# Kernel optimization log

Hardware: AMD Instinct MI355X
Metric: run time of the kernel (lower is better)

Reference implementation:

```python
import jax, jax.numpy as jnp
import numpy as np

P = 2    # padding
R = 2    # ref[0]: rows/cols gathered as conv channels
WP = 3   # ref[1]: conv kernel length along border


def setup_inputs() -> dict:
    key = jax.random.key(0)
    ks = jax.random.split(key, 8)
    B, C, H, W = 8, 128, 256, 256
    HID = 8
    x = jax.random.normal(ks[0], (B, C, H, W), dtype=jnp.float32)
    # stacked params for 4 border MLPs: order top, bottom, left, right
    w1 = jax.random.normal(ks[1], (4, HID, R, WP), dtype=jnp.float32) * 0.3
    b1 = jax.random.normal(ks[2], (4, HID), dtype=jnp.float32) * 0.1
    w2 = jax.random.normal(ks[3], (4, HID, HID), dtype=jnp.float32) * 0.3
    b2 = jax.random.normal(ks[4], (4, HID), dtype=jnp.float32) * 0.1
    w3 = jax.random.normal(ks[5], (4, 1, HID), dtype=jnp.float32) * 0.3
    b3 = jax.random.normal(ks[6], (4, 1), dtype=jnp.float32) * 0.1
    return {"x": x, "w1": w1, "b1": b1, "w2": w2, "b2": b2, "w3": w3, "b3": b3}


def _mlp(slab, w1, b1, w2, b2, w3, b3):
    # slab: (B, R, L, C) -- R gathered lines as channels, L border length, C image channels
    L = slab.shape[2]
    # valid conv along L with WP taps: windows (B, R, WP, L-WP+1, C)
    wins = jnp.stack([slab[:, :, k:L - WP + 1 + k, :] for k in range(WP)], axis=2)
    h = jax.nn.relu(jnp.einsum('brklc,hrk->bhlc', wins, w1) + b1[None, :, None, None])
    h = jax.nn.relu(jnp.einsum('bhlc,gh->bglc', h, w2) + b2[None, :, None, None])
    o = jax.nn.relu(jnp.einsum('bglc,og->bolc', h, w3) + b3[None, :, None, None])
    return o[:, 0]  # (B, L-2, C)


def reference(x, w1, b1, w2, b2, w3, b3):
    B, C, H, W = x.shape
    H2, W2 = H + 2 * P, W + 2 * P
    xp = jnp.zeros((B, C, H2, W2), x.dtype).at[:, :, P:H + P, P:W + P].set(x)
    for i in range(P):
        # top: gather rows [P-i, P-i+R), write row P-1-i, cols 1:W2-1
        top = _mlp(jnp.transpose(xp[:, :, P - i:P + R - i, :], (0, 2, 3, 1)),
                   w1[0], b1[0], w2[0], b2[0], w3[0], b3[0])  # (B, W2-2, C)
        xp = xp.at[:, :, P - 1 - i, 1:W2 - 1].set(jnp.transpose(top, (0, 2, 1)))
        # bottom
        bot = _mlp(jnp.transpose(xp[:, :, H2 - 1 - (R + P) + i:H2 - 1 - P + i, :], (0, 2, 3, 1)),
                   w1[1], b1[1], w2[1], b2[1], w3[1], b3[1])
        xp = xp.at[:, :, H + P + i, 1:W2 - 1].set(jnp.transpose(bot, (0, 2, 1)))
        # left: gather cols, transpose so cols act as channels
        lef = _mlp(jnp.transpose(xp[:, :, :, P - i:P + R - i], (0, 3, 2, 1)),
                   w1[2], b1[2], w2[2], b2[2], w3[2], b3[2])  # (B, H2-2, C)
        xp = xp.at[:, :, 1:H2 - 1, P - 1 - i].set(jnp.transpose(lef, (0, 2, 1)))
        # right
        rig = _mlp(jnp.transpose(xp[:, :, :, W2 - 1 - (R + P) + i:W2 - 1 - P + i], (0, 3, 2, 1)),
                   w1[3], b1[3], w2[3], b2[3], w3[3], b3[3])
        xp = xp.at[:, :, 1:H2 - 1, W + P + i].set(jnp.transpose(rig, (0, 2, 1)))
    return xp
```

## Files before the change

kernel.cpp:

```cpp
#include <hip/hip_runtime.h>


typedef float f32x4 __attribute__((ext_vector_type(4)));
typedef float f32x2 __attribute__((ext_vector_type(2)));

__device__ __forceinline__ int bmap(int r) { return r < 4 ? r : r - 251; }

template <int S>
__device__ __forceinline__ float mlp6(const float* v,
                                      const float* __restrict__ w1, const float* __restrict__ b1,
                                      const float* __restrict__ w2, const float* __restrict__ b2,
                                      const float* __restrict__ w3, const float* __restrict__ b3)
{
    const float* __restrict__ W1 = w1 + S * 48;
    const float* __restrict__ B1 = b1 + S * 8;
    const float* __restrict__ W2 = w2 + S * 64;
    const float* __restrict__ B2 = b2 + S * 8;
    const float* __restrict__ W3 = w3 + S * 8;
    const float  b3s = b3[S];

    float h1[8];
#pragma unroll
    for (int h = 0; h < 8; ++h) {
        float a = B1[h];
#pragma unroll
        for (int q = 0; q < 6; ++q) a = fmaf(v[q], W1[h * 6 + q], a);
        h1[h] = fmaxf(a, 0.f);
    }
    float h2[8];
#pragma unroll
    for (int g = 0; g < 8; ++g) {
        float a = B2[g];
#pragma unroll
        for (int h = 0; h < 8; ++h) a = fmaf(h1[h], W2[g * 8 + h], a);
        h2[g] = fmaxf(a, 0.f);
    }
    float o = b3s;
#pragma unroll
    for (int g = 0; g < 8; ++g) o = fmaf(h2[g], W3[g], o);
    return fmaxf(o, 0.f);
}

template <int S>
__device__ __forceinline__ void hstage(int it, int tid,
                                       float (*rowS)[260], float (*colS)[260],
                                       const float* __restrict__ w1, const float* __restrict__ b1,
                                       const float* __restrict__ w2, const float* __restrict__ b2,
                                       const float* __restrict__ w3, const float* __restrict__ b3)
{
    int rin0, rin1, rout;
    if (S == 0) { rin0 = 2 - it;   rin1 = 3 - it;   rout = 1 - it;   }
    else        { rin0 = 255 + it; rin1 = 256 + it; rout = 258 + it; }
    const int a0 = bmap(rin0), a1 = bmap(rin1), ao = bmap(rout);
    for (int j0 = tid; j0 < 258; j0 += 512) {
        int j = j0 + 1;
        float v[6];
        v[0] = rowS[a0][j - 1]; v[1] = rowS[a0][j]; v[2] = rowS[a0][j + 1];
        v[3] = rowS[a1][j - 1]; v[4] = rowS[a1][j]; v[5] = rowS[a1][j + 1];
        float o = mlp6<S>(v, w1, b1, w2, b2, w3, b3);
        rowS[ao][j] = o;
        if (j < 4 || j >= 255) colS[bmap(j)][rout] = o;
    }
}

template <int S>
__device__ __forceinline__ void vstage(int it, int tid,
                                       float (*rowS)[260], float (*colS)[260],
                                       const float* __restrict__ w1, const float* __restrict__ b1,
                                       const float* __restrict__ w2, const float* __restrict__ b2,
                                       const float* __restrict__ w3, const float* __restrict__ b3)
{
    int cin0, cin1, cout;
    if (S == 2) { cin0 = 2 - it;   cin1 = 3 - it;   cout = 1 - it;   }
    else        { cin0 = 255 + it; cin1 = 256 + it; cout = 258 + it; }
    const int a0 = bmap(cin0), a1 = bmap(cin1), ao = bmap(cout);
    for (int r0 = tid; r0 < 258; r0 += 512) {
        int r = r0 + 1;
        float v[6];
        v[0] = colS[a0][r - 1]; v[1] = colS[a0][r]; v[2] = colS[a0][r + 1];
        v[3] = colS[a1][r - 1]; v[4] = colS[a1][r]; v[5] = colS[a1][r + 1];
        float o = mlp6<S>(v, w1, b1, w2, b2, w3, b3);
        colS[ao][r] = o;
        if (r < 4 || r >= 255) rowS[bmap(r)][cout] = o;
    }
}

__global__ __launch_bounds__(512, 8) void fused_kernel(
    const float* __restrict__ x,
    const float* __restrict__ w1, const float* __restrict__ b1,
    const float* __restrict__ w2, const float* __restrict__ b2,
    const float* __restrict__ w3, const float* __restrict__ b3,
    float* __restrict__ out)
{
    const int tid = threadIdx.x;
    const int bc  = blockIdx.x;
    const float* xs = x + (size_t)bc * 65536;
    float*       os = out + (size_t)bc * 67600;

    __shared__ float rowS[9][260];
    __shared__ float colS[9][260];

    for (int idx = tid; idx < 9 * 260; idx += 512) {
        (&rowS[0][0])[idx] = 0.f;
        (&colS[0][0])[idx] = 0.f;
    }
    __syncthreads();

    for (int idx = tid; idx < 5 * 256; idx += 512) {
        int which = idx >> 8, t = idx & 255;
        int xr = which < 2 ? which : 251 + which;
        rowS[2 + which][2 + t] = xs[xr * 256 + t];
    }
    for (int idx = tid; idx < 5 * 256; idx += 512) {
        int which = idx >> 8, t = idx & 255;
        int xr = which < 2 ? which : 251 + which;
        colS[2 + which][2 + t] = xs[t * 256 + xr];
    }
    __syncthreads();

    for (int it = 0; it < 2; ++it) {
        hstage<0>(it, tid, rowS, colS, w1, b1, w2, b2, w3, b3);
        hstage<1>(it, tid, rowS, colS, w1, b1, w2, b2, w3, b3);
        __syncthreads();
        vstage<2>(it, tid, rowS, colS, w1, b1, w2, b2, w3, b3);
        vstage<3>(it, tid, rowS, colS, w1, b1, w2, b2, w3, b3);
        __syncthreads();
    }

    for (int idx = tid; idx < 4 * 260; idx += 512) {
        int w = idx / 260, cc = idx % 260;
        int rr = w < 2 ? w : 256 + w;
        __builtin_nontemporal_store(rowS[bmap(rr)][cc], &os[(size_t)rr * 260 + cc]);
    }

    for (int idx = tid; idx < 256 * 65; idx += 512) {
        int r = idx / 65;
        int k = idx - r * 65;
        int rp = r + 2;
        float* orow = os + (size_t)rp * 260;
        const float* xrow = xs + (size_t)r * 256;

        f32x4 val;
        if (k == 0) {
            val = (f32x4){colS[0][rp], colS[1][rp], colS[2][rp], colS[3][rp]};
        } else if (k == 64) {
            val = (f32x4){colS[5][rp], colS[6][rp], colS[7][rp], colS[8][rp]};
        } else {
            f32x2 a = __builtin_nontemporal_load((const f32x2*)(xrow + 4 * k - 2));
            f32x2 c = __builtin_nontemporal_load((const f32x2*)(xrow + 4 * k));
            val = (f32x4){a.x, a.y, c.x, c.y};
        }
        __builtin_nontemporal_store(val, (f32x4*)(orow + 4 * k));
    }
}

extern "C" void kernel_launch(void* const* d_in, const int* in_sizes, int n_in,
                              void* d_out, int out_size, void* d_ws, size_t ws_size,
                              hipStream_t stream)
{
    const float* x  = (const float*)d_in[0];
    const float* w1 = (const float*)d_in[1];
    const float* b1 = (const float*)d_in[2];
    const float* w2 = (const float*)d_in[3];
    const float* b2 = (const float*)d_in[4];
    const float* w3 = (const float*)d_in[5];
    const float* b3 = (const float*)d_in[6];
    float* out = (float*)d_out;

    fused_kernel<<<1024, 512, 0, stream>>>(x, w1, b1, w2, b2, w3, b3, out);
}
```

Baseline: 140.1 us.

## Split interior copy and border MLP into separate interleaved blocks

Launches twice as many blocks. Even blocks copy the interior of an image plane, and odd blocks compute the border MLP stages and write only the border columns and rows. The interior copy no longer has to wait behind the serial border computation with its barriers, so memory traffic can overlap with the border compute in other blocks. Nontemporal loads and stores are replaced with plain accesses, and the occupancy hint in launch_bounds is dropped. Each border block still stages the plane's edge rows and columns into shared memory, and the interior edge columns are now written by a different block than the border columns, with the write sets kept disjoint.

Result: slower. 234.2 us (+67.2%).

```diff
diff --git a/kernel.cpp b/kernel.cpp
--- a/kernel.cpp
+++ b/kernel.cpp
@@ -85,7 +85,7 @@
     }
 }
 
-__global__ __launch_bounds__(512, 8) void fused_kernel(
+__global__ __launch_bounds__(512) void padding_kernel(
     const float* __restrict__ x,
     const float* __restrict__ w1, const float* __restrict__ b1,
     const float* __restrict__ w2, const float* __restrict__ b2,
@@ -93,12 +93,32 @@
     float* __restrict__ out)
 {
     const int tid = threadIdx.x;
-    const int bc  = blockIdx.x;
+    const int bc  = blockIdx.x >> 1;
+    const bool is_border = (blockIdx.x & 1) != 0;
     const float* xs = x + (size_t)bc * 65536;
     float*       os = out + (size_t)bc * 67600;
 
     __shared__ float rowS[9][260];
     __shared__ float colS[9][260];
+
+    if (!is_border) {
+        for (int idx = tid; idx < 256 * 65; idx += 512) {
+            int r = idx / 65;
+            int k = idx - r * 65;
+            float*       orow = os + (size_t)(r + 2) * 260;
+            const float* xrow = xs + (size_t)r * 256;
+            if (k == 0) {
+                *(f32x2*)(orow + 2)   = *(const f32x2*)(xrow);
+            } else if (k == 64) {
+                *(f32x2*)(orow + 256) = *(const f32x2*)(xrow + 254);
+            } else {
+                f32x2 a = *(const f32x2*)(xrow + 4 * k - 2);
+                f32x2 c = *(const f32x2*)(xrow + 4 * k);
+                *(f32x4*)(orow + 4 * k) = (f32x4){a.x, a.y, c.x, c.y};
+            }
+        }
+        return;
+    }
 
     for (int idx = tid; idx < 9 * 260; idx += 512) {
         (&rowS[0][0])[idx] = 0.f;
@@ -130,27 +150,14 @@
     for (int idx = tid; idx < 4 * 260; idx += 512) {
         int w = idx / 260, cc = idx % 260;
         int rr = w < 2 ? w : 256 + w;
-        __builtin_nontemporal_store(rowS[bmap(rr)][cc], &os[(size_t)rr * 260 + cc]);
+        os[(size_t)rr * 260 + cc] = rowS[bmap(rr)][cc];
     }
-
-    for (int idx = tid; idx < 256 * 65; idx += 512) {
-        int r = idx / 65;
-        int k = idx - r * 65;
-        int rp = r + 2;
-        float* orow = os + (size_t)rp * 260;
-        const float* xrow = xs + (size_t)r * 256;
-
-        f32x4 val;
-        if (k == 0) {
-            val = (f32x4){colS[0][rp], colS[1][rp], colS[2][rp], colS[3][rp]};
-        } else if (k == 64) {
-            val = (f32x4){colS[5][rp], colS[6][rp], colS[7][rp], colS[8][rp]};
-        } else {
-            f32x2 a = __builtin_nontemporal_load((const f32x2*)(xrow + 4 * k - 2));
-            f32x2 c = __builtin_nontemporal_load((const f32x2*)(xrow + 4 * k));
-            val = (f32x4){a.x, a.y, c.x, c.y};
-        }
-        __builtin_nontemporal_store(val, (f32x4*)(orow + 4 * k));
+    for (int idx = tid; idx < 2 * 256; idx += 512) {
+        int w = idx >> 8;
+        int r = (idx & 255) + 2;
+        float* orow = os + (size_t)r * 260;
+        if (w == 0) *(f32x2*)(orow)       = (f32x2){colS[0][r], colS[1][r]};
+        else        *(f32x2*)(orow + 258) = (f32x2){colS[7][r], colS[8][r]};
     }
 }
 
@@ -167,5 +174,5 @@
     const float* b3 = (const float*)d_in[6];
     float* out = (float*)d_out;
 
-    fused_kernel<<<1024, 512, 0, stream>>>(x, w1, b1, w2, b2, w3, b3, out);
+    padding_kernel<<<2048, 512, 0, stream>>>(x, w1, b1, w2, b2, w3, b3, out);
 }
```
